# Performance work log

Hardware: AMD Instinct MI355X
Metric: run time of the kernel (lower is better)

Reference implementation:

```python
import jax, jax.numpy as jnp
import numpy as np

T, B, E, H = 512, 32, 512, 2048

def setup_inputs() -> dict:
    key = jax.random.key(0)
    k1, k2, k3 = jax.random.split(key, 3)
    sent = jax.random.normal(k1, (T, B, E), dtype=jnp.float32)
    lengths = jax.random.randint(k2, (B,), 1, T + 1)  # unused by the math (pack is never applied)
    # Linear(E, 3H) params (PyTorch default-ish init scale)
    W = jax.random.normal(k3, (3 * H, E), dtype=jnp.float32) * (1.0 / np.sqrt(E))
    b = jnp.zeros((3 * H,), dtype=jnp.float32)
    return {"sent": sent, "lengths": lengths, "W": W, "b": b}

def reference(sent, lengths, W, b):
    # sent: (T, B, E) time-major. Single QRNN layer, window=1, output_gate=True, zoneout=0.
    Y = jnp.einsum('tbe,he->tbh', sent, W) + b          # (T, B, 3H)
    Z, F, O = jnp.split(Y, 3, axis=-1)
    Z = jnp.tanh(Z)
    F = jax.nn.sigmoid(F)
    O = jax.nn.sigmoid(O)

    # forget-mult recurrence: c_t = f_t * z_t + (1 - f_t) * c_{t-1}, c_0 = 0
    def step(c, zf):
        z, f = zf
        c = f * z + (1.0 - f) * c
        return c, c
    c0 = jnp.zeros_like(Z[0])                            # (B, H)
    _, C = jax.lax.scan(step, c0, (Z, F))                # (T, B, H)

    Hseq = O * C                                         # QRNN output (T, B, H)
    embeds = jnp.max(Hseq, axis=0)                       # torch.max(sent_output, 0)[0] -> (B, H)
    return embeds
```

## Files before the change

### kernel.cpp

```cpp
#include <hip/hip_runtime.h>
#include <stdint.h>

#define TT 512
#define BB 32
#define EE 512
#define HH 2048

typedef __attribute__((ext_vector_type(8))) short short8;
typedef __attribute__((ext_vector_type(4))) float f32x4;

#define XROW 528
#define XBUF (16 * XROW)

static __device__ __forceinline__ unsigned short f2bf(float f) {
    union { float f; unsigned u; } v; v.f = f;
    unsigned u = v.u;
    unsigned r = u + 0x7FFFu + ((u >> 16) & 1u);
    return (unsigned short)(r >> 16);
}

static __device__ __forceinline__ float fast_exp(float x) {
    return __builtin_amdgcn_exp2f(x * 1.44269504f);
}
static __device__ __forceinline__ float fast_rcp(float x) {
    return __builtin_amdgcn_rcpf(x);
}

static __device__ __forceinline__ void load_lds16(const unsigned short* g, unsigned short* l) {
    __builtin_amdgcn_global_load_lds(
        (const __attribute__((address_space(1))) unsigned int*)(uintptr_t)g,
        (__attribute__((address_space(3))) unsigned int*)(uintptr_t)l,
        16, 0, 0);
}

__global__ void convert_inputs(const float* __restrict__ X,
                               const float* __restrict__ W,
                               unsigned short* __restrict__ Xb,
                               unsigned short* __restrict__ Wb) {
    const int nX = TT * BB * EE;
    int i = (blockIdx.x * blockDim.x + threadIdx.x) * 8;
    const float* src;
    unsigned short* dst;
    int j;
    if (i < nX) { src = X; dst = Xb; j = i; }
    else        { src = W; dst = Wb; j = i - nX; }
    float4 v0 = *(const float4*)(src + j);
    float4 v1 = *(const float4*)(src + j + 4);
    union { short8 s; unsigned short u[8]; } o;
    o.u[0] = f2bf(v0.x); o.u[1] = f2bf(v0.y); o.u[2] = f2bf(v0.z); o.u[3] = f2bf(v0.w);
    o.u[4] = f2bf(v1.x); o.u[5] = f2bf(v1.y); o.u[6] = f2bf(v1.z); o.u[7] = f2bf(v1.w);
    *(short8*)(dst + j) = o.s;
}

__launch_bounds__(256, 2)
__global__ void qrnn_fused(const unsigned short* __restrict__ Xb,
                           const unsigned short* __restrict__ Wb,
                           const float* __restrict__ bias,
                           float* __restrict__ out)
{
    __shared__ unsigned short xlds[2 * XBUF];
    __shared__ float exch[2][2][64][12];

    const int tid  = threadIdx.x;
    const int wv   = tid >> 6;
    const int lane = tid & 63;
    const int q    = lane >> 4;
    const int c    = lane & 15;
    const int hi   = wv >> 1;
    const int s    = wv & 1;

    const int id   = blockIdx.x;
    const int xcd  = id & 7;
    const int slot = id >> 3;
    const int b    = xcd * 4 + (slot >> 6);
    const int hgrp = slot & 63;
    const int h    = hgrp * 32 + hi * 16 + c;

    short8 wz[8], wf[8], wo[8];
    {
        const unsigned short* wzr = Wb + (size_t)h * EE            + s * 256;
        const unsigned short* wfr = Wb + (size_t)(HH + h) * EE     + s * 256;
        const unsigned short* wor = Wb + (size_t)(2 * HH + h) * EE + s * 256;
#pragma unroll
        for (int k = 0; k < 8; ++k) {
            int e0 = k * 32 + q * 8;
            wz[k] = *(const short8*)(wzr + e0);
            wf[k] = *(const short8*)(wfr + e0);
            wo[k] = *(const short8*)(wor + e0);
        }
    }
#pragma unroll
    for (int k = 0; k < 8; ++k) {
        asm volatile("" : "+a"(wz[k]), "+a"(wf[k]), "+a"(wo[k]));
    }

    const float b0 = (s == 0) ? bias[h]          : 0.0f;
    const float b1 = (s == 0) ? bias[HH + h]     : 0.0f;
    const float b2 = (s == 0) ? bias[2 * HH + h] : 0.0f;

    float carry = 0.0f;
    float vmax  = -1e30f;

    const unsigned short* g0 = Xb + ((size_t)(wv * 4) * BB + b) * EE + lane * 8;
    unsigned short* l0 = &xlds[(wv * 4) * XROW];

    auto stage = [&](int n, int slt) {
        const unsigned short* g = g0 + (size_t)n * (16 * BB * EE);
        unsigned short* l = l0 + slt * XBUF;
#pragma unroll
        for (int i = 0; i < 4; ++i)
            load_lds16(g + (size_t)i * (BB * EE), l + i * XROW);
    };

    auto do_tail = [&](f32x4 az, f32x4 af, f32x4 ao) {
        float aa[4], mm[4], oo[4];
#pragma unroll
        for (int r = 0; r < 4; ++r) {
            float e2 = fast_exp(2.0f * az[r]);
            float z  = 1.0f - 2.0f * fast_rcp(e2 + 1.0f);
            float f  = fast_rcp(1.0f + fast_exp(-af[r]));
            float o  = fast_rcp(1.0f + fast_exp(-ao[r]));
            aa[r] = f * z;
            mm[r] = 1.0f - f;
            oo[r] = o;
        }

        float A = aa[0], M = mm[0];
#pragma unroll
        for (int r = 1; r < 4; ++r) { A = aa[r] + mm[r] * A; M = mm[r] * M; }

        float Ap = __shfl_up(A, 16, 64), Mp = __shfl_up(M, 16, 64);
        if (q >= 1) { A = A + M * Ap; M = M * Mp; }
        Ap = __shfl_up(A, 32, 64); Mp = __shfl_up(M, 32, 64);
        if (q >= 2) { A = A + M * Ap; M = M * Mp; }
        float Ae = __shfl_up(A, 16, 64), Me = __shfl_up(M, 16, 64);
        if (q == 0) { Ae = 0.0f; Me = 1.0f; }
        float cc = Ae + Me * carry;

#pragma unroll
        for (int r = 0; r < 4; ++r) {
            cc = aa[r] + mm[r] * cc;
            vmax = fmaxf(vmax, oo[r] * cc);
        }

        float cend = A + M * carry;
        carry = __shfl(cend, 48 + c, 64);
    };

    stage(0, 0);
    __syncthreads();

    f32x4 prevz, prevf, prevo;

    for (int ch = 0; ch < 32; ++ch) {
        const int buf = ch & 1;
        if (ch < 31) stage(ch + 1, buf ^ 1);

        const unsigned short* Abase = &xlds[buf * XBUF + c * XROW + s * 256 + q * 8];
        short8 a[8];
#pragma unroll
        for (int k = 0; k < 8; ++k)
            a[k] = *(const short8*)(Abase + k * 32);

        f32x4 pz, pf, po;
        if (s == 0 && ch > 0) {
            const float* e = &exch[(ch - 1) & 1][hi][lane][0];
            pz = *(const f32x4*)(e);
            pf = *(const f32x4*)(e + 4);
            po = *(const f32x4*)(e + 8);
        }

        f32x4 az = {b0, b0, b0, b0};
        f32x4 af = {b1, b1, b1, b1};
        f32x4 ao = {b2, b2, b2, b2};
#pragma unroll
        for (int k = 0; k < 8; ++k) {
            az = __builtin_amdgcn_mfma_f32_16x16x32_bf16(a[k], wz[k], az, 0, 0, 0);
            af = __builtin_amdgcn_mfma_f32_16x16x32_bf16(a[k], wf[k], af, 0, 0, 0);
            ao = __builtin_amdgcn_mfma_f32_16x16x32_bf16(a[k], wo[k], ao, 0, 0, 0);
        }

        if (s == 1) {
            float* e = &exch[ch & 1][hi][lane][0];
            *(f32x4*)(e)     = az;
            *(f32x4*)(e + 4) = af;
            *(f32x4*)(e + 8) = ao;
        }

        if (s == 0 && ch > 0) {
            do_tail(prevz + pz, prevf + pf, prevo + po);
        }

        prevz = az; prevf = af; prevo = ao;

        __syncthreads();
    }

    if (s == 0) {
        const float* e = &exch[31 & 1][hi][lane][0];
        f32x4 pz = *(const f32x4*)(e);
        f32x4 pf = *(const f32x4*)(e + 4);
        f32x4 po = *(const f32x4*)(e + 8);
        do_tail(prevz + pz, prevf + pf, prevo + po);

        vmax = fmaxf(vmax, __shfl_xor(vmax, 16, 64));
        vmax = fmaxf(vmax, __shfl_xor(vmax, 32, 64));
        if (q == 0) out[(size_t)b * HH + h] = vmax;
    }
}

extern "C" void kernel_launch(void* const* d_in, const int* in_sizes, int n_in,
                              void* d_out, int out_size, void* d_ws, size_t ws_size,
                              hipStream_t stream) {
    const float* sent = (const float*)d_in[0];
    const float* W    = (const float*)d_in[2];
    const float* bias = (const float*)d_in[3];
    float* out        = (float*)d_out;

    const int nX = TT * BB * EE;
    const int nW = 3 * HH * EE;
    unsigned short* Xb = (unsigned short*)d_ws;
    unsigned short* Wb = Xb + nX;

    int totalVec = (nX + nW) / 8;
    convert_inputs<<<totalVec / 256, 256, 0, stream>>>(sent, W, Xb, Wb);

    dim3 grid(2048);
    qrnn_fused<<<grid, 256, 0, stream>>>(Xb, Wb, bias, out);
}
```

Measured before the change: 236.9 us.

## Split activation and scan across wave pairs; use hardware bf16 pack conversion

The fused kernel now splits the per-chunk tail across the two K-half waves. The s=1 wave sums the partial accumulators and computes tanh/sigmoid into a new LDS buffer. The s=0 wave runs the serial scan on activations from two chunks earlier, so transcendental work and the scan are pipelined rather than serialized on one wave. The conversion kernel uses v_cvt_pk_bf16_f32 with a grid-stride loop over a fixed 2048 blocks, and barriers become explicit waitcnt+s_barrier. This adds LDS traffic and a second exchange buffer, and lengthens the pipeline by one chunk.

```diff
diff --git a/kernel.cpp b/kernel.cpp
--- a/kernel.cpp
+++ b/kernel.cpp
@@ -12,18 +12,19 @@
 #define XROW 528
 #define XBUF (16 * XROW)
 
-static __device__ __forceinline__ unsigned short f2bf(float f) {
-    union { float f; unsigned u; } v; v.f = f;
-    unsigned u = v.u;
-    unsigned r = u + 0x7FFFu + ((u >> 16) & 1u);
-    return (unsigned short)(r >> 16);
-}
+#define BAR_VM0() asm volatile("s_waitcnt vmcnt(0) lgkmcnt(0)\n\ts_barrier" ::: "memory")
 
 static __device__ __forceinline__ float fast_exp(float x) {
     return __builtin_amdgcn_exp2f(x * 1.44269504f);
 }
 static __device__ __forceinline__ float fast_rcp(float x) {
     return __builtin_amdgcn_rcpf(x);
+}
+
+static __device__ __forceinline__ unsigned cvtpk_bf16(float lo, float hi) {
+    unsigned r;
+    asm("v_cvt_pk_bf16_f32 %0, %1, %2" : "=v"(r) : "v"(lo), "v"(hi));
+    return r;
 }
 
 static __device__ __forceinline__ void load_lds16(const unsigned short* g, unsigned short* l) {
@@ -38,18 +39,24 @@
                                unsigned short* __restrict__ Xb,
                                unsigned short* __restrict__ Wb) {
     const int nX = TT * BB * EE;
-    int i = (blockIdx.x * blockDim.x + threadIdx.x) * 8;
-    const float* src;
-    unsigned short* dst;
-    int j;
-    if (i < nX) { src = X; dst = Xb; j = i; }
-    else        { src = W; dst = Wb; j = i - nX; }
-    float4 v0 = *(const float4*)(src + j);
-    float4 v1 = *(const float4*)(src + j + 4);
-    union { short8 s; unsigned short u[8]; } o;
-    o.u[0] = f2bf(v0.x); o.u[1] = f2bf(v0.y); o.u[2] = f2bf(v0.z); o.u[3] = f2bf(v0.w);
-    o.u[4] = f2bf(v1.x); o.u[5] = f2bf(v1.y); o.u[6] = f2bf(v1.z); o.u[7] = f2bf(v1.w);
-    *(short8*)(dst + j) = o.s;
+    const int nT = (nX + 3 * HH * EE) / 8;
+    const int stride = gridDim.x * blockDim.x;
+    for (int g = blockIdx.x * blockDim.x + threadIdx.x; g < nT; g += stride) {
+        int i = g * 8;
+        const float* src;
+        unsigned short* dst;
+        int j;
+        if (i < nX) { src = X; dst = Xb; j = i; }
+        else        { src = W; dst = Wb; j = i - nX; }
+        float4 v0 = *(const float4*)(src + j);
+        float4 v1 = *(const float4*)(src + j + 4);
+        union { short8 s; unsigned u[4]; } o;
+        o.u[0] = cvtpk_bf16(v0.x, v0.y);
+        o.u[1] = cvtpk_bf16(v0.z, v0.w);
+        o.u[2] = cvtpk_bf16(v1.x, v1.y);
+        o.u[3] = cvtpk_bf16(v1.z, v1.w);
+        *(short8*)(dst + j) = o.s;
+    }
 }
 
 __launch_bounds__(256, 2)
@@ -59,7 +66,8 @@
                            float* __restrict__ out)
 {
     __shared__ unsigned short xlds[2 * XBUF];
-    __shared__ float exch[2][2][64][12];
+    __shared__ float rawx[2][2][64][12];
+    __shared__ float actx[2][2][64][12];
 
     const int tid  = threadIdx.x;
     const int wv   = tid >> 6;
@@ -94,9 +102,9 @@
         asm volatile("" : "+a"(wz[k]), "+a"(wf[k]), "+a"(wo[k]));
     }
 
-    const float b0 = (s == 0) ? bias[h]          : 0.0f;
-    const float b1 = (s == 0) ? bias[HH + h]     : 0.0f;
-    const float b2 = (s == 0) ? bias[2 * HH + h] : 0.0f;
+    const float b0 = bias[h];
+    const float b1 = bias[HH + h];
+    const float b2 = bias[2 * HH + h];
 
     float carry = 0.0f;
     float vmax  = -1e30f;
@@ -112,17 +120,31 @@
             load_lds16(g + (size_t)i * (BB * EE), l + i * XROW);
     };
 
-    auto do_tail = [&](f32x4 az, f32x4 af, f32x4 ao) {
+    auto do_act = [&](int n, f32x4 sz, f32x4 sf, f32x4 so) {
+        float* e = &actx[n & 1][hi][lane][0];
+#pragma unroll
+        for (int r = 0; r < 4; ++r) {
+            float zz = sz[r] + b0;
+            float ff = sf[r] + b1;
+            float oo = so[r] + b2;
+            float e2 = fast_exp(2.0f * zz);
+            float z  = 1.0f - 2.0f * fast_rcp(e2 + 1.0f);
+            float f  = fast_rcp(1.0f + fast_exp(-ff));
+            float o  = fast_rcp(1.0f + fast_exp(-oo));
+            e[r]     = f * z;
+            e[4 + r] = 1.0f - f;
+            e[8 + r] = o;
+        }
+    };
+
+    auto do_scan = [&](int n) {
+        const float* e = &actx[n & 1][hi][lane][0];
         float aa[4], mm[4], oo[4];
 #pragma unroll
         for (int r = 0; r < 4; ++r) {
-            float e2 = fast_exp(2.0f * az[r]);
-            float z  = 1.0f - 2.0f * fast_rcp(e2 + 1.0f);
-            float f  = fast_rcp(1.0f + fast_exp(-af[r]));
-            float o  = fast_rcp(1.0f + fast_exp(-ao[r]));
-            aa[r] = f * z;
-            mm[r] = 1.0f - f;
-            oo[r] = o;
+            aa[r] = e[r];
+            mm[r] = e[4 + r];
+            oo[r] = e[8 + r];
         }
 
         float A = aa[0], M = mm[0];
@@ -148,7 +170,7 @@
     };
 
     stage(0, 0);
-    __syncthreads();
+    BAR_VM0();
 
     f32x4 prevz, prevf, prevo;
 
@@ -162,17 +184,9 @@
         for (int k = 0; k < 8; ++k)
             a[k] = *(const short8*)(Abase + k * 32);
 
-        f32x4 pz, pf, po;
-        if (s == 0 && ch > 0) {
-            const float* e = &exch[(ch - 1) & 1][hi][lane][0];
-            pz = *(const f32x4*)(e);
-            pf = *(const f32x4*)(e + 4);
-            po = *(const f32x4*)(e + 8);
-        }
-
-        f32x4 az = {b0, b0, b0, b0};
-        f32x4 af = {b1, b1, b1, b1};
-        f32x4 ao = {b2, b2, b2, b2};
+        f32x4 az = {0.f, 0.f, 0.f, 0.f};
+        f32x4 af = {0.f, 0.f, 0.f, 0.f};
+        f32x4 ao = {0.f, 0.f, 0.f, 0.f};
 #pragma unroll
         for (int k = 0; k < 8; ++k) {
             az = __builtin_amdgcn_mfma_f32_16x16x32_bf16(a[k], wz[k], az, 0, 0, 0);
@@ -180,28 +194,39 @@
             ao = __builtin_amdgcn_mfma_f32_16x16x32_bf16(a[k], wo[k], ao, 0, 0, 0);
         }
 
-        if (s == 1) {
-            float* e = &exch[ch & 1][hi][lane][0];
+        if (s == 0) {
+            float* e = &rawx[ch & 1][hi][lane][0];
             *(f32x4*)(e)     = az;
             *(f32x4*)(e + 4) = af;
             *(f32x4*)(e + 8) = ao;
-        }
-
-        if (s == 0 && ch > 0) {
-            do_tail(prevz + pz, prevf + pf, prevo + po);
-        }
-
-        prevz = az; prevf = af; prevo = ao;
-
-        __syncthreads();
-    }
+
+            if (ch > 1) do_scan(ch - 2);
+        } else {
+            if (ch > 0) {
+                const float* e = &rawx[(ch - 1) & 1][hi][lane][0];
+                f32x4 sz = prevz + *(const f32x4*)(e);
+                f32x4 sf = prevf + *(const f32x4*)(e + 4);
+                f32x4 so = prevo + *(const f32x4*)(e + 8);
+                do_act(ch - 1, sz, sf, so);
+            }
+            prevz = az; prevf = af; prevo = ao;
+        }
+
+        BAR_VM0();
+    }
+
+    if (s == 1) {
+        const float* e = &rawx[31 & 1][hi][lane][0];
+        f32x4 sz = prevz + *(const f32x4*)(e);
+        f32x4 sf = prevf + *(const f32x4*)(e + 4);
+        f32x4 so = prevo + *(const f32x4*)(e + 8);
+        do_act(31, sz, sf, so);
+    }
+    BAR_VM0();
 
     if (s == 0) {
-        const float* e = &exch[31 & 1][hi][lane][0];
-        f32x4 pz = *(const f32x4*)(e);
-        f32x4 pf = *(const f32x4*)(e + 4);
-        f32x4 po = *(const f32x4*)(e + 8);
-        do_tail(prevz + pz, prevf + pf, prevo + po);
+        do_scan(30);
+        do_scan(31);
 
         vmax = fmaxf(vmax, __shfl_xor(vmax, 16, 64));
         vmax = fmaxf(vmax, __shfl_xor(vmax, 32, 64));
@@ -222,8 +247,7 @@
     unsigned short* Xb = (unsigned short*)d_ws;
     unsigned short* Wb = Xb + nX;
 
-    int totalVec = (nX + nW) / 8;
-    convert_inputs<<<totalVec / 256, 256, 0, stream>>>(sent, W, Xb, Wb);
+    convert_inputs<<<2048, 256, 0, stream>>>(sent, W, Xb, Wb);
 
     dim3 grid(2048);
     qrnn_fused<<<grid, 256, 0, stream>>>(Xb, Wb, bias, out);
```

Measured after the change: 238.3 us. No clear change (+0.6%).
